# Kernel tuning notes

Measured on AMD Instinct MI355X. Metric: run time of the kernel, lower is better.

The kernel has to match this reference:

```python
import jax, jax.numpy as jnp
import numpy as np

N = 4096          # flattened batch*seq tokens
V = 32000         # tgt_vocab_size
LS = 0.1          # label_smoothing
CONF = 1.0 - LS   # confidence mass on gold token
SM = LS / (V - 1) # smoothing mass per non-gold token
IGNORE = -1
PAD = 0


def setup_inputs() -> dict:
    key = jax.random.key(0)
    k1, k2 = jax.random.split(key)
    output = jax.random.normal(k1, (N, V), dtype=jnp.float32)
    target = jax.random.randint(k2, (N,), 0, V, dtype=jnp.int32)
    return {"output": output, "target": target}


def reference(output, target):
    n, v = output.shape
    valid = (target != IGNORE)                       # all True for generated data; kept for fidelity
    tgt = jnp.where(valid, target, PAD)
    validf = valid.astype(output.dtype)
    rows = jnp.arange(n)

    # label-smoothed KL term
    logp = jax.nn.log_softmax(output, axis=-1)       # (N, V)
    model_prob = jnp.full((n, v), SM, dtype=logp.dtype).at[rows, tgt].set(CONF)
    kl_row = jnp.sum(model_prob * (jnp.log(model_prob) - logp), axis=-1)
    loss = jnp.sum(kl_row * validf)

    # unlikelihood term: previous-context tokens as negative candidates
    full = jnp.broadcast_to(tgt[None, :], (n, n))    # (N, N)
    ctx_l = jnp.tril(full, -1)                       # strictly-lower = preceding targets
    ctx_u = ctx_l + PAD
    ctx_u = ctx_u * jnp.triu(ctx_u)                  # faithful to torch construction
    ctx = ctx_l + ctx_u
    ctx = jnp.where(ctx == tgt[:, None], PAD, ctx)   # don't penalize the gold token
    neg = jnp.zeros((n, v), dtype=logp.dtype).at[rows[:, None], ctx].set(1.0)
    neg = neg.at[:, PAD].set(0.0)                    # (N, V) negative-target mask

    one_minus = jnp.clip(1.0 - jnp.exp(logp), 1e-5, None)
    custom_row = jnp.sum(-jnp.log(one_minus) * neg, axis=-1)
    custom = jnp.sum(custom_row * validf)

    norm = jnp.sum((valid & (tgt != PAD)).astype(logp.dtype))
    return loss / norm + 0.1 * custom / norm
```

## Files before the change

### kernel.cpp

```cpp
#include <hip/hip_runtime.h>
#include <math.h>

#define NROWS 4096
#define VCOLS 32000
#define NV4   (VCOLS / 4)

constexpr float CONF_F   = 0.9f;
constexpr float SM_F     = 0.1f / 31999.0f;
constexpr float KL_CONST = -1.36242896f;
constexpr float COEF_T   = CONF_F - SM_F;

__global__ void k_init(int* __restrict__ ft32) {
    int v = blockIdx.x * blockDim.x + threadIdx.x;
    if (v < VCOLS) ft32[v] = NROWS;
}

__global__ void k_scatter(const int* __restrict__ target,
                          int* __restrict__ ft32,
                          int* __restrict__ tclean) {
    int j = blockIdx.x * blockDim.x + threadIdx.x;
    if (j < NROWS) {
        int t  = target[j];
        int tc = (t != -1) ? t : 0;
        tclean[j] = tc;
        if (tc != 0) atomicMin(&ft32[tc], j);
    }
}

__global__ void k_pack(const int* __restrict__ ft32,
                       unsigned short* __restrict__ ft16) {
    int v = blockIdx.x * blockDim.x + threadIdx.x;
    if (v < VCOLS) ft16[v] = (unsigned short)ft32[v];
}

__global__ __launch_bounds__(256)
void k_main(const float* __restrict__ X,
            const int*   __restrict__ target,
            const int*   __restrict__ tclean,
            const unsigned short* __restrict__ ft16,
            float* __restrict__ kl_rows,
            float* __restrict__ custom_rows) {
    const int i   = blockIdx.x;
    const int tid = threadIdx.x;

    __shared__ float cand[NROWS];
    __shared__ float rm[256], rz[256], rs[256];
    __shared__ float s_logZ, s_xt;

    const bool valid = (target[i] != -1);
    if (!valid) {
        if (tid == 0) { kl_rows[i] = 0.0f; custom_rows[i] = 0.0f; }
        return;
    }

    const int    mytgt = tclean[i];
    const float* row   = X + (size_t)i * VCOLS;

    for (int j = tid; j < i; j += 256) cand[j] = -INFINITY;
    __syncthreads();

    const float4* row4 = (const float4*)row;
    const int2*   ft2  = (const int2*)ft16;

    float m = -INFINITY, Z = 0.0f, sx = 0.0f;

#define MAX4(xx) fmaxf(fmaxf((xx).x, (xx).y), fmaxf((xx).z, (xx).w))
#define PROC(xx, ff, ee) do {                                                \
        Z  += __expf((xx).x - m) + __expf((xx).y - m)                        \
            + __expf((xx).z - m) + __expf((xx).w - m);                       \
        sx += ((xx).x + (xx).y) + ((xx).z + (xx).w);                         \
        int base_ = (ee) * 4;                                                \
        int a0_ = (ff).x & 0xFFFF, a1_ = (int)(((unsigned)(ff).x) >> 16);    \
        int a2_ = (ff).y & 0xFFFF, a3_ = (int)(((unsigned)(ff).y) >> 16);    \
        unsigned d_ = (unsigned)(mytgt - base_);                             \
        if (a0_ < i && d_ != 0u) cand[a0_] = (xx).x;                         \
        if (a1_ < i && d_ != 1u) cand[a1_] = (xx).y;                         \
        if (a2_ < i && d_ != 2u) cand[a2_] = (xx).z;                         \
        if (a3_ < i && d_ != 3u) cand[a3_] = (xx).w;                         \
        if (d_ < 4u) s_xt = (d_ == 0u) ? (xx).x : (d_ == 1u) ? (xx).y        \
                          : (d_ == 2u) ? (xx).z : (xx).w;                    \
    } while (0)

    for (int eb = tid; eb < NV4; eb += 1024) {
        const bool v1 = (eb +  256) < NV4;
        const bool v2 = (eb +  512) < NV4;
        const bool v3 = (eb +  768) < NV4;
        float4 x0, x1, x2, x3;
        int2   f0, f1, f2, f3;
        x0 = row4[eb];              f0 = ft2[eb];
        if (v1) { x1 = row4[eb + 256]; f1 = ft2[eb + 256]; }
        if (v2) { x2 = row4[eb + 512]; f2 = ft2[eb + 512]; }
        if (v3) { x3 = row4[eb + 768]; f3 = ft2[eb + 768]; }

        float cm = MAX4(x0);
        if (v1) cm = fmaxf(cm, MAX4(x1));
        if (v2) cm = fmaxf(cm, MAX4(x2));
        if (v3) cm = fmaxf(cm, MAX4(x3));
        if (cm > m) { Z *= __expf(m - cm); m = cm; }

        PROC(x0, f0, eb);
        if (v1) PROC(x1, f1, eb + 256);
        if (v2) PROC(x2, f2, eb + 512);
        if (v3) PROC(x3, f3, eb + 768);
    }
#undef PROC
#undef MAX4

    rm[tid] = m; rz[tid] = Z; rs[tid] = sx;
    __syncthreads();
    for (int s = 128; s > 0; s >>= 1) {
        if (tid < s) {
            float m2 = rm[tid + s], z2 = rz[tid + s];
            float mm = fmaxf(rm[tid], m2);
            rz[tid]  = rz[tid] * __expf(rm[tid] - mm) + z2 * __expf(m2 - mm);
            rm[tid]  = mm;
            rs[tid] += rs[tid + s];
        }
        __syncthreads();
    }
    if (tid == 0) {
        float logZ    = rm[0] + __logf(rz[0]);
        s_logZ        = logZ;
        float logp_t  = s_xt - logZ;
        float sumlogp = rs[0] - (float)VCOLS * logZ;
        kl_rows[i] = KL_CONST - COEF_T * logp_t - SM_F * sumlogp;
    }
    __syncthreads();
    const float logZ = s_logZ;

    float acc = 0.0f;
    for (int j = tid; j < i; j += 256) {
        float xv = cand[j];
        float p  = __expf(xv - logZ);
        float om = fmaxf(1.0f - p, 1e-5f);
        acc -= __logf(om);
    }
    rs[tid] = acc;
    __syncthreads();
    for (int s = 128; s > 0; s >>= 1) {
        if (tid < s) rs[tid] += rs[tid + s];
        __syncthreads();
    }
    if (tid == 0) custom_rows[i] = rs[0];
}

__global__ void k_final(const float* __restrict__ kl_rows,
                        const float* __restrict__ custom_rows,
                        const int*   __restrict__ target,
                        float* __restrict__ out) {
    __shared__ float sl[256], sc[256], sn[256];
    int tid = threadIdx.x;
    float L = 0.0f, C = 0.0f, Nn = 0.0f;
    for (int j = tid; j < NROWS; j += 256) {
        L += kl_rows[j];
        C += custom_rows[j];
        int t = target[j];
        if (t != -1 && t != 0) Nn += 1.0f;
    }
    sl[tid] = L; sc[tid] = C; sn[tid] = Nn;
    __syncthreads();
    for (int s = 128; s > 0; s >>= 1) {
        if (tid < s) { sl[tid] += sl[tid+s]; sc[tid] += sc[tid+s]; sn[tid] += sn[tid+s]; }
        __syncthreads();
    }
    if (tid == 0) {
        float norm = sn[0];
        out[0] = sl[0] / norm + 0.1f * sc[0] / norm;
    }
}

extern "C" void kernel_launch(void* const* d_in, const int* in_sizes, int n_in,
                              void* d_out, int out_size, void* d_ws, size_t ws_size,
                              hipStream_t stream) {
    const float* X      = (const float*)d_in[0];
    const int*   target = (const int*)d_in[1];
    float*       out    = (float*)d_out;

    char* ws = (char*)d_ws;
    int*            ft32        = (int*)           (ws);
    unsigned short* ft16        = (unsigned short*)(ws + 128000);
    int*            tclean      = (int*)           (ws + 192000);
    float*          kl_rows     = (float*)         (ws + 192000 + 16384);
    float*          custom_rows = (float*)         (ws + 192000 + 32768);

    k_init   <<<(VCOLS + 255) / 256, 256, 0, stream>>>(ft32);
    k_scatter<<<(NROWS + 255) / 256, 256, 0, stream>>>(target, ft32, tclean);
    k_pack   <<<(VCOLS + 255) / 256, 256, 0, stream>>>(ft32, ft16);
    k_main   <<<NROWS,               256, 0, stream>>>(X, target, tclean, ft16,
                                                       kl_rows, custom_rows);
    k_final  <<<1,                   256, 0, stream>>>(kl_rows, custom_rows, target, out);
}
```

Before: 116.4 us.

## Fuse final reduction into main kernel via last-block ticket

Removes the separate final reduction kernel by having each block take an atomic ticket, with the last finishing block performing the global reduction. It also drops the tclean buffer by reading target directly, loads the gold logit with a single scalar read instead of a per-element select, and makes the online-max rescale branchless. This saves one kernel launch and some per-element work, at the cost of an atomic plus threadfence per block.

```diff
diff --git a/kernel.cpp b/kernel.cpp
--- a/kernel.cpp
+++ b/kernel.cpp
@@ -4,25 +4,26 @@
 #define NROWS 4096
 #define VCOLS 32000
 #define NV4   (VCOLS / 4)
+
+typedef float f32x4 __attribute__((ext_vector_type(4)));
 
 constexpr float CONF_F   = 0.9f;
 constexpr float SM_F     = 0.1f / 31999.0f;
 constexpr float KL_CONST = -1.36242896f;
 constexpr float COEF_T   = CONF_F - SM_F;
 
-__global__ void k_init(int* __restrict__ ft32) {
+__global__ void k_init(int* __restrict__ ft32, int* __restrict__ ticket) {
     int v = blockIdx.x * blockDim.x + threadIdx.x;
     if (v < VCOLS) ft32[v] = NROWS;
+    if (v == 0)    *ticket = 0;
 }
 
 __global__ void k_scatter(const int* __restrict__ target,
-                          int* __restrict__ ft32,
-                          int* __restrict__ tclean) {
+                          int* __restrict__ ft32) {
     int j = blockIdx.x * blockDim.x + threadIdx.x;
     if (j < NROWS) {
         int t  = target[j];
         int tc = (t != -1) ? t : 0;
-        tclean[j] = tc;
         if (tc != 0) atomicMin(&ft32[tc], j);
     }
 }
@@ -36,136 +37,146 @@
 __global__ __launch_bounds__(256)
 void k_main(const float* __restrict__ X,
             const int*   __restrict__ target,
-            const int*   __restrict__ tclean,
             const unsigned short* __restrict__ ft16,
             float* __restrict__ kl_rows,
-            float* __restrict__ custom_rows) {
+            float* __restrict__ custom_rows,
+            int*   __restrict__ ticket,
+            float* __restrict__ out) {
     const int i   = blockIdx.x;
     const int tid = threadIdx.x;
 
     __shared__ float cand[NROWS];
     __shared__ float rm[256], rz[256], rs[256];
     __shared__ float s_logZ, s_xt;
-
-    const bool valid = (target[i] != -1);
-    if (!valid) {
-        if (tid == 0) { kl_rows[i] = 0.0f; custom_rows[i] = 0.0f; }
-        return;
-    }
-
-    const int    mytgt = tclean[i];
-    const float* row   = X + (size_t)i * VCOLS;
-
-    for (int j = tid; j < i; j += 256) cand[j] = -INFINITY;
-    __syncthreads();
-
-    const float4* row4 = (const float4*)row;
-    const int2*   ft2  = (const int2*)ft16;
-
-    float m = -INFINITY, Z = 0.0f, sx = 0.0f;
-
-#define MAX4(xx) fmaxf(fmaxf((xx).x, (xx).y), fmaxf((xx).z, (xx).w))
-#define PROC(xx, ff, ee) do {                                                \
-        Z  += __expf((xx).x - m) + __expf((xx).y - m)                        \
-            + __expf((xx).z - m) + __expf((xx).w - m);                       \
-        sx += ((xx).x + (xx).y) + ((xx).z + (xx).w);                         \
-        int base_ = (ee) * 4;                                                \
-        int a0_ = (ff).x & 0xFFFF, a1_ = (int)(((unsigned)(ff).x) >> 16);    \
-        int a2_ = (ff).y & 0xFFFF, a3_ = (int)(((unsigned)(ff).y) >> 16);    \
-        unsigned d_ = (unsigned)(mytgt - base_);                             \
-        if (a0_ < i && d_ != 0u) cand[a0_] = (xx).x;                         \
-        if (a1_ < i && d_ != 1u) cand[a1_] = (xx).y;                         \
-        if (a2_ < i && d_ != 2u) cand[a2_] = (xx).z;                         \
-        if (a3_ < i && d_ != 3u) cand[a3_] = (xx).w;                         \
-        if (d_ < 4u) s_xt = (d_ == 0u) ? (xx).x : (d_ == 1u) ? (xx).y        \
-                          : (d_ == 2u) ? (xx).z : (xx).w;                    \
+    __shared__ int   s_last;
+
+    const int t = target[i];
+    const bool valid = (t != -1);
+
+    if (valid) {
+        const int    mytgt = t;
+        const float* row   = X + (size_t)i * VCOLS;
+
+        if (tid == 0) s_xt = row[mytgt];
+        for (int j = tid; j < i; j += 256) cand[j] = -INFINITY;
+        __syncthreads();
+
+        const f32x4* row4 = (const f32x4*)row;
+        const int2*  ft2  = (const int2*)ft16;
+
+        float m = -INFINITY, Z = 0.0f, sx = 0.0f;
+
+#define MAX4(xx_) fmaxf(fmaxf((xx_).x, (xx_).y), fmaxf((xx_).z, (xx_).w))
+#define PROC(xx_, ff_, ee_) do {                                              \
+        Z += __expf((xx_).x - m) + __expf((xx_).y - m)                        \
+           + __expf((xx_).z - m) + __expf((xx_).w - m);                       \
+        sx += ((xx_).x + (xx_).y) + ((xx_).z + (xx_).w);                      \
+        int base_ = (ee_) * 4;                                                \
+        int a0_ = (ff_).x & 0xFFFF, a1_ = (int)(((unsigned)(ff_).x) >> 16);   \
+        int a2_ = (ff_).y & 0xFFFF, a3_ = (int)(((unsigned)(ff_).y) >> 16);   \
+        unsigned d_ = (unsigned)(mytgt - base_);                              \
+        if (a0_ < i && d_ != 0u) cand[a0_] = (xx_).x;                         \
+        if (a1_ < i && d_ != 1u) cand[a1_] = (xx_).y;                         \
+        if (a2_ < i && d_ != 2u) cand[a2_] = (xx_).z;                         \
+        if (a3_ < i && d_ != 3u) cand[a3_] = (xx_).w;                         \
     } while (0)
 
-    for (int eb = tid; eb < NV4; eb += 1024) {
-        const bool v1 = (eb +  256) < NV4;
-        const bool v2 = (eb +  512) < NV4;
-        const bool v3 = (eb +  768) < NV4;
-        float4 x0, x1, x2, x3;
-        int2   f0, f1, f2, f3;
-        x0 = row4[eb];              f0 = ft2[eb];
-        if (v1) { x1 = row4[eb + 256]; f1 = ft2[eb + 256]; }
-        if (v2) { x2 = row4[eb + 512]; f2 = ft2[eb + 512]; }
-        if (v3) { x3 = row4[eb + 768]; f3 = ft2[eb + 768]; }
-
-        float cm = MAX4(x0);
-        if (v1) cm = fmaxf(cm, MAX4(x1));
-        if (v2) cm = fmaxf(cm, MAX4(x2));
-        if (v3) cm = fmaxf(cm, MAX4(x3));
-        if (cm > m) { Z *= __expf(m - cm); m = cm; }
-
-        PROC(x0, f0, eb);
-        if (v1) PROC(x1, f1, eb + 256);
-        if (v2) PROC(x2, f2, eb + 512);
-        if (v3) PROC(x3, f3, eb + 768);
-    }
+        for (int eb = tid; eb < NV4; eb += 1024) {
+            const bool v1 = (eb +  256) < NV4;
+            const bool v2 = (eb +  512) < NV4;
+            const bool v3 = (eb +  768) < NV4;
+            f32x4 x0, x1, x2, x3;
+            int2  f0, f1, f2, f3;
+            x0 = row4[eb];                 f0 = ft2[eb];
+            if (v1) { x1 = row4[eb + 256]; f1 = ft2[eb + 256]; }
+            if (v2) { x2 = row4[eb + 512]; f2 = ft2[eb + 512]; }
+            if (v3) { x3 = row4[eb + 768]; f3 = ft2[eb + 768]; }
+
+            float cm = MAX4(x0);
+            if (v1) cm = fmaxf(cm, MAX4(x1));
+            if (v2) cm = fmaxf(cm, MAX4(x2));
+            if (v3) cm = fmaxf(cm, MAX4(x3));
+            float mn = fmaxf(m, cm);
+            Z *= __expf(m - mn);
+            m  = mn;
+
+            PROC(x0, f0, eb);
+            if (v1) PROC(x1, f1, eb + 256);
+            if (v2) PROC(x2, f2, eb + 512);
+            if (v3) PROC(x3, f3, eb + 768);
+        }
 #undef PROC
 #undef MAX4
 
-    rm[tid] = m; rz[tid] = Z; rs[tid] = sx;
+        rm[tid] = m; rz[tid] = Z; rs[tid] = sx;
+        __syncthreads();
+        for (int s = 128; s > 0; s >>= 1) {
+            if (tid < s) {
+                float m2 = rm[tid + s], z2 = rz[tid + s];
+                float mm = fmaxf(rm[tid], m2);
+                rz[tid]  = rz[tid] * __expf(rm[tid] - mm) + z2 * __expf(m2 - mm);
+                rm[tid]  = mm;
+                rs[tid] += rs[tid + s];
+            }
+            __syncthreads();
+        }
+        if (tid == 0) {
+            float logZ    = rm[0] + __logf(rz[0]);
+            s_logZ        = logZ;
+            float logp_t  = s_xt - logZ;
+            float sumlogp = rs[0] - (float)VCOLS * logZ;
+            kl_rows[i] = KL_CONST - COEF_T * logp_t - SM_F * sumlogp;
+        }
+        __syncthreads();
+        const float logZ = s_logZ;
+
+        float acc = 0.0f;
+        for (int j = tid; j < i; j += 256) {
+            float xv = cand[j];
+            float p  = __expf(xv - logZ);
+            float om = fmaxf(1.0f - p, 1e-5f);
+            acc -= __logf(om);
+        }
+        rs[tid] = acc;
+        __syncthreads();
+        for (int s = 128; s > 0; s >>= 1) {
+            if (tid < s) rs[tid] += rs[tid + s];
+            __syncthreads();
+        }
+        if (tid == 0) custom_rows[i] = rs[0];
+    } else {
+        if (tid == 0) { kl_rows[i] = 0.0f; custom_rows[i] = 0.0f; }
+    }
+
     __syncthreads();
-    for (int s = 128; s > 0; s >>= 1) {
-        if (tid < s) {
-            float m2 = rm[tid + s], z2 = rz[tid + s];
-            float mm = fmaxf(rm[tid], m2);
-            rz[tid]  = rz[tid] * __expf(rm[tid] - mm) + z2 * __expf(m2 - mm);
-            rm[tid]  = mm;
-            rs[tid] += rs[tid + s];
-        }
-        __syncthreads();
-    }
     if (tid == 0) {
-        float logZ    = rm[0] + __logf(rz[0]);
-        s_logZ        = logZ;
-        float logp_t  = s_xt - logZ;
-        float sumlogp = rs[0] - (float)VCOLS * logZ;
-        kl_rows[i] = KL_CONST - COEF_T * logp_t - SM_F * sumlogp;
+        __threadfence();
+        s_last = (atomicAdd(ticket, 1) == NROWS - 1);
     }
     __syncthreads();
-    const float logZ = s_logZ;
-
-    float acc = 0.0f;
-    for (int j = tid; j < i; j += 256) {
-        float xv = cand[j];
-        float p  = __expf(xv - logZ);
-        float om = fmaxf(1.0f - p, 1e-5f);
-        acc -= __logf(om);
-    }
-    rs[tid] = acc;
-    __syncthreads();
-    for (int s = 128; s > 0; s >>= 1) {
-        if (tid < s) rs[tid] += rs[tid + s];
-        __syncthreads();
-    }
-    if (tid == 0) custom_rows[i] = rs[0];
-}
-
-__global__ void k_final(const float* __restrict__ kl_rows,
-                        const float* __restrict__ custom_rows,
-                        const int*   __restrict__ target,
-                        float* __restrict__ out) {
-    __shared__ float sl[256], sc[256], sn[256];
-    int tid = threadIdx.x;
-    float L = 0.0f, C = 0.0f, Nn = 0.0f;
-    for (int j = tid; j < NROWS; j += 256) {
-        L += kl_rows[j];
-        C += custom_rows[j];
-        int t = target[j];
-        if (t != -1 && t != 0) Nn += 1.0f;
-    }
-    sl[tid] = L; sc[tid] = C; sn[tid] = Nn;
-    __syncthreads();
-    for (int s = 128; s > 0; s >>= 1) {
-        if (tid < s) { sl[tid] += sl[tid+s]; sc[tid] += sc[tid+s]; sn[tid] += sn[tid+s]; }
-        __syncthreads();
-    }
-    if (tid == 0) {
-        float norm = sn[0];
-        out[0] = sl[0] / norm + 0.1f * sc[0] / norm;
+    if (s_last) {
+        __threadfence();
+        float L = 0.0f, C = 0.0f, Nn = 0.0f;
+        for (int j = tid; j < NROWS; j += 256) {
+            L += kl_rows[j];
+            C += custom_rows[j];
+            int tj = target[j];
+            if (tj != -1 && tj != 0) Nn += 1.0f;
+        }
+        rm[tid] = L; rz[tid] = C; rs[tid] = Nn;
+        __syncthreads();
+        for (int s = 128; s > 0; s >>= 1) {
+            if (tid < s) {
+                rm[tid] += rm[tid + s];
+                rz[tid] += rz[tid + s];
+                rs[tid] += rs[tid + s];
+            }
+            __syncthreads();
+        }
+        if (tid == 0) {
+            float norm = rs[0];
+            out[0] = rm[0] / norm + 0.1f * rz[0] / norm;
+        }
     }
 }
 
@@ -179,14 +190,14 @@
     char* ws = (char*)d_ws;
     int*            ft32        = (int*)           (ws);
     unsigned short* ft16        = (unsigned short*)(ws + 128000);
-    int*            tclean      = (int*)           (ws + 192000);
-    float*          kl_rows     = (float*)         (ws + 192000 + 16384);
-    float*          custom_rows = (float*)         (ws + 192000 + 32768);
-
-    k_init   <<<(VCOLS + 255) / 256, 256, 0, stream>>>(ft32);
-    k_scatter<<<(NROWS + 255) / 256, 256, 0, stream>>>(target, ft32, tclean);
+    float*          kl_rows     = (float*)         (ws + 192000);
+    float*          custom_rows = (float*)         (ws + 192000 + 16384);
+    int*            ticket      = (int*)           (ws + 192000 + 32768);
+
+    k_init   <<<(VCOLS + 255) / 256, 256, 0, stream>>>(ft32, ticket);
+    k_scatter<<<(NROWS + 255) / 256, 256, 0, stream>>>(target, ft32);
     k_pack   <<<(VCOLS + 255) / 256, 256, 0, stream>>>(ft32, ft16);
-    k_main   <<<NROWS,               256, 0, stream>>>(X, target, tclean, ft16,
-                                                       kl_rows, custom_rows);
-    k_final  <<<1,                   256, 0, stream>>>(kl_rows, custom_rows, target, out);
-}
+    k_main   <<<NROWS,               256, 0, stream>>>(X, target, ft16,
+                                                       kl_rows, custom_rows,
+                                                       ticket, out);
+}
```

New measurement: 314.9 us. 171% more time.
